# Performance work log

Measured on AMD Instinct MI355X. Metric: run time of the kernel, lower is better.

## Reference

```python
import jax, jax.numpy as jnp
import numpy as np

N_HEAD = 12

def setup_inputs() -> dict:
    key = jax.random.key(0)
    ks = jax.random.split(key, 5)
    B, T, C = 1, 4096, 768
    scale = 0.02
    return {
        "x": jax.random.normal(ks[0], (B, T, C), jnp.float32),
        "w_attn": jax.random.normal(ks[1], (C, 3 * C), jnp.float32) * scale,
        "b_attn": jax.random.normal(ks[2], (3 * C,), jnp.float32) * scale,
        "w_proj": jax.random.normal(ks[3], (C, C), jnp.float32) * scale,
        "b_proj": jax.random.normal(ks[4], (C,), jnp.float32) * scale,
    }

def reference(x, w_attn, b_attn, w_proj, b_proj):
    B, T, C = x.shape
    H = N_HEAD
    D = C // H
    qkv = x @ w_attn + b_attn                      # [B,T,3C]
    q, k, v = jnp.split(qkv, 3, axis=-1)
    # [B,T,C] -> [B,H,T,D]
    q = q.reshape(B, T, H, D).transpose(0, 2, 1, 3)
    k = k.reshape(B, T, H, D).transpose(0, 2, 1, 3)
    v = v.reshape(B, T, H, D).transpose(0, 2, 1, 3)
    att = jnp.einsum("bhqd,bhkd->bhqk", q, k) * (1.0 / np.sqrt(D))
    causal = jnp.tril(jnp.ones((T, T), bool))
    att = jnp.where(causal[None, None], att, -jnp.inf)
    att = jax.nn.softmax(att, axis=-1)
    y = jnp.einsum("bhqk,bhkd->bhqd", att, v)      # [B,H,T,D]
    y = y.transpose(0, 2, 1, 3).reshape(B, T, C)
    return y @ w_proj + b_proj
```

## Files before the change

### kernel.cpp

```cpp
#include <hip/hip_runtime.h>
#include <hip/hip_bf16.h>
#include <cstdint>
#include <cstddef>

#define NHEAD 12
#define TSEQ  4096
#define CDIM  768

typedef __attribute__((ext_vector_type(8))) short bf16x8;
typedef __attribute__((ext_vector_type(4))) float f32x4;
typedef __attribute__((ext_vector_type(16))) float f32x16;
typedef __attribute__((ext_vector_type(2))) unsigned int u32x2;

typedef __attribute__((address_space(1))) void gvoid;
typedef __attribute__((address_space(3))) void lvoid;

#define QSCALE 0.1803368801111204f

static __device__ __forceinline__ unsigned short f2bf(float f) {
    union { float f; uint32_t u; } v; v.f = f;
    uint32_t u = v.u;
    u += 0x7fffu + ((u >> 16) & 1u);
    return (unsigned short)(u >> 16);
}

static __device__ __forceinline__ f32x4 mfma16(bf16x8 a, bf16x8 b, f32x4 c) {
    return __builtin_amdgcn_mfma_f32_16x16x32_bf16(a, b, c, 0, 0, 0);
}
static __device__ __forceinline__ f32x16 mfma32(bf16x8 a, bf16x8 b, f32x16 c) {
    return __builtin_amdgcn_mfma_f32_32x32x16_bf16(a, b, c, 0, 0, 0);
}
static __device__ __forceinline__ unsigned cvt_pk_bf16(float lo, float hi) {
    unsigned r;
    asm("v_cvt_pk_bf16_f32 %0, %1, %2" : "=v"(r) : "v"(lo), "v"(hi));
    return r;
}


__global__ void cvt_f32_bf16(const float* __restrict__ in, unsigned short* __restrict__ out, int n4) {
    int i = blockIdx.x * blockDim.x + threadIdx.x;
    int stride = gridDim.x * blockDim.x;
    for (int idx = i; idx < n4; idx += stride) {
        float4 v = reinterpret_cast<const float4*>(in)[idx];
        ushort4 o;
        o.x = f2bf(v.x); o.y = f2bf(v.y); o.z = f2bf(v.z); o.w = f2bf(v.w);
        reinterpret_cast<ushort4*>(out)[idx] = o;
    }
}

__global__ void transpose_cvt(const float* __restrict__ W, unsigned short* __restrict__ Wt,
                              int K, int N) {
    __shared__ float tile[32][33];
    int n0 = blockIdx.x * 32;
    int k0 = blockIdx.y * 32;
    int tx = threadIdx.x & 31;
    int ty = threadIdx.x >> 5;
    #pragma unroll
    for (int r = ty; r < 32; r += 8)
        tile[r][tx] = W[(size_t)(k0 + r) * N + n0 + tx];
    __syncthreads();
    #pragma unroll
    for (int r = ty; r < 32; r += 8)
        Wt[(size_t)(n0 + r) * K + k0 + tx] = f2bf(tile[tx][r]);
}


template<int MODE>
__global__ __launch_bounds__(256)
void gemm_bt(const unsigned short* __restrict__ A,
             const unsigned short* __restrict__ Bt,
             const float* __restrict__ bias,
             unsigned short* __restrict__ Qb,
             unsigned short* __restrict__ Kb,
             unsigned short* __restrict__ Vt,
             float* __restrict__ Out,
             int M, int N, int K)
{
    __shared__ __align__(16) unsigned short As[128 * 32];
    __shared__ __align__(16) unsigned short Bs[128 * 32];

    const int tid  = threadIdx.x;
    const int lane = tid & 63;
    const int w    = tid >> 6;
    const int wr   = w >> 1, wc = w & 1;
    const int row0 = blockIdx.x * 128;
    const int col0 = blockIdx.y * 128;
    const int l16  = lane & 15;
    const int lhi  = lane >> 4;

    f32x4 acc[4][4] = {};

    for (int k0 = 0; k0 < K; k0 += 32) {
        __syncthreads();
        #pragma unroll
        for (int r = 0; r < 2; ++r) {
            int b    = r * 4096 + w * 1024 + lane * 16;
            int trow = b >> 6;
            int koff = b & 63;
            const char* gA = (const char*)A  + ((size_t)(row0 + trow) * K + k0) * 2 + koff;
            const char* gB = (const char*)Bt + ((size_t)(col0 + trow) * K + k0) * 2 + koff;
            __builtin_amdgcn_global_load_lds((gvoid*)gA,
                (lvoid*)((char*)As + r * 4096 + w * 1024), 16, 0, 0);
            __builtin_amdgcn_global_load_lds((gvoid*)gB,
                (lvoid*)((char*)Bs + r * 4096 + w * 1024), 16, 0, 0);
        }
        __syncthreads();

        bf16x8 a[4], bfr[4];
        #pragma unroll
        for (int m = 0; m < 4; ++m) {
            int row = wr * 64 + m * 16 + l16;
            a[m] = *reinterpret_cast<const bf16x8*>(&As[row * 32 + lhi * 8]);
        }
        #pragma unroll
        for (int n = 0; n < 4; ++n) {
            int col = wc * 64 + n * 16 + l16;
            bfr[n] = *reinterpret_cast<const bf16x8*>(&Bs[col * 32 + lhi * 8]);
        }
        #pragma unroll
        for (int m = 0; m < 4; ++m)
            #pragma unroll
            for (int n = 0; n < 4; ++n)
                acc[m][n] = mfma16(a[m], bfr[n], acc[m][n]);
    }

    #pragma unroll
    for (int m = 0; m < 4; ++m) {
        int trow = row0 + wr * 64 + m * 16 + lhi * 4;
        #pragma unroll
        for (int n = 0; n < 4; ++n) {
            int ncol = col0 + wc * 64 + n * 16 + l16;
            float bv = bias[ncol];
            #pragma unroll
            for (int j = 0; j < 4; ++j) {
                float v = acc[m][n][j] + bv;
                int t = trow + j;
                if (MODE == 0) {
                    if (ncol < 768) {
                        int hh = ncol >> 6, d = ncol & 63;
                        Qb[((size_t)hh * TSEQ + t) * 64 + d] = f2bf(v * QSCALE);
                    } else if (ncol < 1536) {
                        int c = ncol - 768; int hh = c >> 6, d = c & 63;
                        Kb[((size_t)hh * TSEQ + t) * 64 + d] = f2bf(v);
                    } else {
                        int c = ncol - 1536; int hh = c >> 6, d = c & 63;
                        Vt[((size_t)hh * 64 + d) * TSEQ + t] = f2bf(v);
                    }
                } else {
                    Out[(size_t)t * N + ncol] = v;
                }
            }
        }
    }
}


__global__ __launch_bounds__(256, 3)
void attn_fwd(const unsigned short* __restrict__ Qb,
              const unsigned short* __restrict__ Kb,
              const unsigned short* __restrict__ Vt,
              unsigned short* __restrict__ Y)
{
    __shared__ __align__(16) float Osh[3][32][64];
    __shared__ float Msh[3][64];
    __shared__ float Lsh[3][64];

    const int tid  = threadIdx.x;
    const int lane = tid & 63;
    const int w    = tid >> 6;
    const int l31  = lane & 31;
    const int hi   = lane >> 5;
    const int bid  = blockIdx.x;
    const int h    = bid % NHEAD;
    const int qb   = 127 - bid / NHEAD;
    const int q0   = qb * 32;
    const int ntiles = q0 / 64 + 1;

    const unsigned short* Qh = Qb + (size_t)h * TSEQ * 64;
    const unsigned short* Kh = Kb + (size_t)h * TSEQ * 64;
    const unsigned short* Vh = Vt + (size_t)h * 64 * TSEQ;

    bf16x8 qf[4];
    #pragma unroll
    for (int ks = 0; ks < 4; ++ks)
        qf[ks] = *reinterpret_cast<const bf16x8*>(
            &Qh[(size_t)(q0 + l31) * 64 + ks * 16 + hi * 8]);

    f32x16 o0 = {}, o1 = {};
    float mrun = -1e30f, lrun = 0.f;

    for (int kt = w; kt < ntiles; kt += 4) {
        const int kv0 = kt * 64;

        bf16x8 kf[2][4];
        #pragma unroll
        for (int sub = 0; sub < 2; ++sub)
            #pragma unroll
            for (int ks = 0; ks < 4; ++ks)
                kf[sub][ks] = *reinterpret_cast<const bf16x8*>(
                    &Kh[(size_t)(kv0 + sub * 32 + l31) * 64 + ks * 16 + hi * 8]);

        bf16x8 vf[2][4];
        #pragma unroll
        for (int d = 0; d < 2; ++d)
            #pragma unroll
            for (int ks = 0; ks < 4; ++ks)
                vf[d][ks] = *reinterpret_cast<const bf16x8*>(
                    &Vh[(size_t)(d * 32 + l31) * TSEQ + kv0 + ks * 16 + hi * 8]);

        f32x16 s0 = {}, s1 = {};
        #pragma unroll
        for (int ks = 0; ks < 4; ++ks) {
            s0 = mfma32(kf[0][ks], qf[ks], s0);
            s1 = mfma32(kf[1][ks], qf[ks], s1);
        }

        float sv[32];
        #pragma unroll
        for (int i = 0; i < 16; ++i) { sv[i] = s0[i]; sv[16 + i] = s1[i]; }

        if (kt == ntiles - 1) {
            const int qrel = q0 + l31 - kv0;
            const int h4 = hi * 4;
            #pragma unroll
            for (int i = 0; i < 32; ++i) {
                int kvbase = (i >> 4) * 32 + (i & 3) + 8 * ((i >> 2) & 3);
                if (kvbase + h4 > qrel) sv[i] = -1e30f;
            }
        }

        float t[16];
        #pragma unroll
        for (int i = 0; i < 16; ++i) t[i] = fmaxf(sv[i], sv[i + 16]);
        #pragma unroll
        for (int s = 8; s >= 1; s >>= 1)
            #pragma unroll
            for (int i = 0; i < s; ++i) t[i] = fmaxf(t[i], t[i + s]);
        float pmax;
        {
            union { float f; unsigned u; } c; c.f = t[0];
            u32x2 r = __builtin_amdgcn_permlane32_swap(c.u, c.u, false, false);
            union { unsigned u; float f; } ra, rb; ra.u = r.x; rb.u = r.y;
            pmax = fmaxf(ra.f, rb.f);
        }

        if (!__all(pmax <= mrun + 8.0f)) {
            float mnew = fmaxf(mrun, pmax);
            float corr = exp2f(mrun - mnew);
            #pragma unroll
            for (int i = 0; i < 16; ++i) { o0[i] *= corr; o1[i] *= corr; }
            lrun *= corr;
            mrun = mnew;
        }

        float e[32];
        #pragma unroll
        for (int i = 0; i < 32; ++i) e[i] = exp2f(sv[i] - mrun);

        float u[16];
        #pragma unroll
        for (int i = 0; i < 16; ++i) u[i] = e[i] + e[i + 16];
        #pragma unroll
        for (int s = 8; s >= 1; s >>= 1)
            #pragma unroll
            for (int i = 0; i < s; ++i) u[i] += u[i + s];
        float ps;
        {
            union { float f; unsigned u; } c; c.f = u[0];
            u32x2 r = __builtin_amdgcn_permlane32_swap(c.u, c.u, false, false);
            union { unsigned u; float f; } ra, rb; ra.u = r.x; rb.u = r.y;
            ps = ra.f + rb.f;
        }
        lrun += ps;

        bf16x8 pw[4];
        #pragma unroll
        for (int ks = 0; ks < 4; ++ks) {
            const int eb = (ks >> 1) * 16 + (ks & 1) * 8;
            u32x2 r02 = __builtin_amdgcn_permlane32_swap(
                cvt_pk_bf16(e[eb + 0], e[eb + 1]), cvt_pk_bf16(e[eb + 4], e[eb + 5]),
                false, false);
            u32x2 r13 = __builtin_amdgcn_permlane32_swap(
                cvt_pk_bf16(e[eb + 2], e[eb + 3]), cvt_pk_bf16(e[eb + 6], e[eb + 7]),
                false, false);
            union { unsigned wd[4]; bf16x8 v; } pk;
            pk.wd[0] = r02.x; pk.wd[1] = r13.x; pk.wd[2] = r02.y; pk.wd[3] = r13.y;
            pw[ks] = pk.v;
        }

        #pragma unroll
        for (int ks = 0; ks < 4; ++ks) {
            o0 = mfma32(vf[0][ks], pw[ks], o0);
            o1 = mfma32(vf[1][ks], pw[ks], o1);
        }
    }

    if (w > 0) {
        #pragma unroll
        for (int i = 0; i < 16; ++i) {
            Osh[w - 1][i][lane]      = o0[i];
            Osh[w - 1][16 + i][lane] = o1[i];
        }
        Msh[w - 1][lane] = mrun;
        Lsh[w - 1][lane] = lrun;
    }
    __syncthreads();
    if (w == 0) {
        #pragma unroll
        for (int p = 0; p < 3; ++p) {
            float mp = Msh[p][lane], lp = Lsh[p][lane];
            float mn = fmaxf(mrun, mp);
            float a = exp2f(mrun - mn), b = exp2f(mp - mn);
            #pragma unroll
            for (int i = 0; i < 16; ++i) {
                o0[i] = o0[i] * a + Osh[p][i][lane] * b;
                o1[i] = o1[i] * a + Osh[p][16 + i][lane] * b;
            }
            lrun = lrun * a + lp * b;
            mrun = mn;
        }

        float inv = 1.0f / lrun;
        const int trow = q0 + l31;
        #pragma unroll
        for (int d = 0; d < 2; ++d) {
            #pragma unroll
            for (int p = 0; p < 8; ++p) {
                const int rr = p * 2;
                float v0 = (d ? o1 : o0)[rr] * inv;
                float v1 = (d ? o1 : o0)[rr + 1] * inv;
                int c = h * 64 + d * 32 + (rr & 3) + 8 * (rr >> 2) + hi * 4;
                unsigned wd = cvt_pk_bf16(v0, v1);
                *reinterpret_cast<unsigned*>(
                    const_cast<unsigned short*>(&Y[(size_t)trow * CDIM + c])) = wd;
            }
        }
    }
}


extern "C" void kernel_launch(void* const* d_in, const int* in_sizes, int n_in,
                              void* d_out, int out_size, void* d_ws, size_t ws_size,
                              hipStream_t stream) {
    const float* x      = (const float*)d_in[0];
    const float* w_attn = (const float*)d_in[1];
    const float* b_attn = (const float*)d_in[2];
    const float* w_proj = (const float*)d_in[3];
    const float* b_proj = (const float*)d_in[4];
    float* out = (float*)d_out;

    char* ws = (char*)d_ws;
    unsigned short* xb  = (unsigned short*)(ws + 0);
    unsigned short* WaT = (unsigned short*)(ws + 6291456);
    unsigned short* WpT = (unsigned short*)(ws + 9830400);
    unsigned short* Qb  = (unsigned short*)(ws + 11010048);
    unsigned short* Kb  = (unsigned short*)(ws + 17301504);
    unsigned short* Vt  = (unsigned short*)(ws + 23592960);
    unsigned short* Yb  = (unsigned short*)(ws + 29884416);

    cvt_f32_bf16<<<2048, 256, 0, stream>>>(x, xb, TSEQ * CDIM / 4);
    transpose_cvt<<<dim3(2304 / 32, 768 / 32), 256, 0, stream>>>(w_attn, WaT, 768, 2304);
    transpose_cvt<<<dim3(768 / 32, 768 / 32), 256, 0, stream>>>(w_proj, WpT, 768, 768);

    gemm_bt<0><<<dim3(TSEQ / 128, 2304 / 128), 256, 0, stream>>>(
        xb, WaT, b_attn, Qb, Kb, Vt, nullptr, TSEQ, 2304, CDIM);

    attn_fwd<<<NHEAD * (TSEQ / 32), 256, 0, stream>>>(Qb, Kb, Vt, Yb);

    gemm_bt<1><<<dim3(TSEQ / 128, CDIM / 128), 256, 0, stream>>>(
        Yb, WpT, b_proj, nullptr, nullptr, nullptr, out, TSEQ, CDIM, CDIM);
}
```

Before: 231.4 us.

## Pair causal query blocks per attention workgroup and split KV across eight waves

Each attention workgroup now handles two 32-row query blocks, a long one (127-pair) and a short one (pair), so every block gets a similar amount of causal work. The grid shrinks to 768 blocks of 512 threads. Within a block the KV tiles are split across eight waves instead of four, and the partial softmax states are merged through shared memory in two stages. The aim is better load balance and more waves per KV sweep, at the cost of extra barriers, a larger shared-memory footprint, and a launch bound of 512 threads with 5 blocks that may tighten the register budget.

```diff
diff --git a/kernel.cpp b/kernel.cpp
--- a/kernel.cpp
+++ b/kernel.cpp
@@ -155,15 +155,15 @@
 }
 
 
-__global__ __launch_bounds__(256, 3)
+__global__ __launch_bounds__(512, 5)
 void attn_fwd(const unsigned short* __restrict__ Qb,
               const unsigned short* __restrict__ Kb,
               const unsigned short* __restrict__ Vt,
               unsigned short* __restrict__ Y)
 {
-    __shared__ __align__(16) float Osh[3][32][64];
-    __shared__ float Msh[3][64];
-    __shared__ float Lsh[3][64];
+    __shared__ __align__(16) float Osh[4][32][64];
+    __shared__ float Msh[4][64];
+    __shared__ float Lsh[4][64];
 
     const int tid  = threadIdx.x;
     const int lane = tid & 63;
@@ -172,167 +172,196 @@
     const int hi   = lane >> 5;
     const int bid  = blockIdx.x;
     const int h    = bid % NHEAD;
-    const int qb   = 127 - bid / NHEAD;
-    const int q0   = qb * 32;
-    const int ntiles = q0 / 64 + 1;
+    const int pair = bid / NHEAD;
 
     const unsigned short* Qh = Qb + (size_t)h * TSEQ * 64;
     const unsigned short* Kh = Kb + (size_t)h * TSEQ * 64;
     const unsigned short* Vh = Vt + (size_t)h * 64 * TSEQ;
 
-    bf16x8 qf[4];
-    #pragma unroll
-    for (int ks = 0; ks < 4; ++ks)
-        qf[ks] = *reinterpret_cast<const bf16x8*>(
-            &Qh[(size_t)(q0 + l31) * 64 + ks * 16 + hi * 8]);
-
-    f32x16 o0 = {}, o1 = {};
-    float mrun = -1e30f, lrun = 0.f;
-
-    for (int kt = w; kt < ntiles; kt += 4) {
-        const int kv0 = kt * 64;
-
-        bf16x8 kf[2][4];
-        #pragma unroll
-        for (int sub = 0; sub < 2; ++sub)
-            #pragma unroll
-            for (int ks = 0; ks < 4; ++ks)
-                kf[sub][ks] = *reinterpret_cast<const bf16x8*>(
-                    &Kh[(size_t)(kv0 + sub * 32 + l31) * 64 + ks * 16 + hi * 8]);
-
-        bf16x8 vf[2][4];
-        #pragma unroll
-        for (int d = 0; d < 2; ++d)
-            #pragma unroll
-            for (int ks = 0; ks < 4; ++ks)
-                vf[d][ks] = *reinterpret_cast<const bf16x8*>(
-                    &Vh[(size_t)(d * 32 + l31) * TSEQ + kv0 + ks * 16 + hi * 8]);
-
-        f32x16 s0 = {}, s1 = {};
-        #pragma unroll
-        for (int ks = 0; ks < 4; ++ks) {
-            s0 = mfma32(kf[0][ks], qf[ks], s0);
-            s1 = mfma32(kf[1][ks], qf[ks], s1);
-        }
-
-        float sv[32];
-        #pragma unroll
-        for (int i = 0; i < 16; ++i) { sv[i] = s0[i]; sv[16 + i] = s1[i]; }
-
-        if (kt == ntiles - 1) {
-            const int qrel = q0 + l31 - kv0;
-            const int h4 = hi * 4;
-            #pragma unroll
-            for (int i = 0; i < 32; ++i) {
-                int kvbase = (i >> 4) * 32 + (i & 3) + 8 * ((i >> 2) & 3);
-                if (kvbase + h4 > qrel) sv[i] = -1e30f;
-            }
-        }
-
-        float t[16];
-        #pragma unroll
-        for (int i = 0; i < 16; ++i) t[i] = fmaxf(sv[i], sv[i + 16]);
-        #pragma unroll
-        for (int s = 8; s >= 1; s >>= 1)
-            #pragma unroll
-            for (int i = 0; i < s; ++i) t[i] = fmaxf(t[i], t[i + s]);
-        float pmax;
-        {
-            union { float f; unsigned u; } c; c.f = t[0];
-            u32x2 r = __builtin_amdgcn_permlane32_swap(c.u, c.u, false, false);
-            union { unsigned u; float f; } ra, rb; ra.u = r.x; rb.u = r.y;
-            pmax = fmaxf(ra.f, rb.f);
-        }
-
-        if (!__all(pmax <= mrun + 8.0f)) {
-            float mnew = fmaxf(mrun, pmax);
-            float corr = exp2f(mrun - mnew);
-            #pragma unroll
-            for (int i = 0; i < 16; ++i) { o0[i] *= corr; o1[i] *= corr; }
-            lrun *= corr;
-            mrun = mnew;
-        }
-
-        float e[32];
-        #pragma unroll
-        for (int i = 0; i < 32; ++i) e[i] = exp2f(sv[i] - mrun);
-
-        float u[16];
-        #pragma unroll
-        for (int i = 0; i < 16; ++i) u[i] = e[i] + e[i + 16];
-        #pragma unroll
-        for (int s = 8; s >= 1; s >>= 1)
-            #pragma unroll
-            for (int i = 0; i < s; ++i) u[i] += u[i + s];
-        float ps;
-        {
-            union { float f; unsigned u; } c; c.f = u[0];
-            u32x2 r = __builtin_amdgcn_permlane32_swap(c.u, c.u, false, false);
-            union { unsigned u; float f; } ra, rb; ra.u = r.x; rb.u = r.y;
-            ps = ra.f + rb.f;
-        }
-        lrun += ps;
-
-        bf16x8 pw[4];
-        #pragma unroll
-        for (int ks = 0; ks < 4; ++ks) {
-            const int eb = (ks >> 1) * 16 + (ks & 1) * 8;
-            u32x2 r02 = __builtin_amdgcn_permlane32_swap(
-                cvt_pk_bf16(e[eb + 0], e[eb + 1]), cvt_pk_bf16(e[eb + 4], e[eb + 5]),
-                false, false);
-            u32x2 r13 = __builtin_amdgcn_permlane32_swap(
-                cvt_pk_bf16(e[eb + 2], e[eb + 3]), cvt_pk_bf16(e[eb + 6], e[eb + 7]),
-                false, false);
-            union { unsigned wd[4]; bf16x8 v; } pk;
-            pk.wd[0] = r02.x; pk.wd[1] = r13.x; pk.wd[2] = r02.y; pk.wd[3] = r13.y;
-            pw[ks] = pk.v;
-        }
-
-        #pragma unroll
-        for (int ks = 0; ks < 4; ++ks) {
-            o0 = mfma32(vf[0][ks], pw[ks], o0);
-            o1 = mfma32(vf[1][ks], pw[ks], o1);
-        }
-    }
-
-    if (w > 0) {
-        #pragma unroll
-        for (int i = 0; i < 16; ++i) {
-            Osh[w - 1][i][lane]      = o0[i];
-            Osh[w - 1][16 + i][lane] = o1[i];
-        }
-        Msh[w - 1][lane] = mrun;
-        Lsh[w - 1][lane] = lrun;
-    }
-    __syncthreads();
-    if (w == 0) {
-        #pragma unroll
-        for (int p = 0; p < 3; ++p) {
-            float mp = Msh[p][lane], lp = Lsh[p][lane];
+    #pragma unroll 1
+    for (int phase = 0; phase < 2; ++phase) {
+        const int qblk = phase ? pair : (127 - pair);
+        const int q0   = qblk * 32;
+        const int ntiles = q0 / 64 + 1;
+
+        bf16x8 qf[4];
+        #pragma unroll
+        for (int ks = 0; ks < 4; ++ks)
+            qf[ks] = *reinterpret_cast<const bf16x8*>(
+                &Qh[(size_t)(q0 + l31) * 64 + ks * 16 + hi * 8]);
+
+        f32x16 o0 = {}, o1 = {};
+        float mrun = -1e30f, lrun = 0.f;
+
+        for (int kt = w; kt < ntiles; kt += 8) {
+            const int kv0 = kt * 64;
+
+            bf16x8 kf[2][4];
+            #pragma unroll
+            for (int sub = 0; sub < 2; ++sub)
+                #pragma unroll
+                for (int ks = 0; ks < 4; ++ks)
+                    kf[sub][ks] = *reinterpret_cast<const bf16x8*>(
+                        &Kh[(size_t)(kv0 + sub * 32 + l31) * 64 + ks * 16 + hi * 8]);
+
+            bf16x8 vf[2][4];
+            #pragma unroll
+            for (int d = 0; d < 2; ++d)
+                #pragma unroll
+                for (int ks = 0; ks < 4; ++ks)
+                    vf[d][ks] = *reinterpret_cast<const bf16x8*>(
+                        &Vh[(size_t)(d * 32 + l31) * TSEQ + kv0 + ks * 16 + hi * 8]);
+
+            f32x16 s0 = {}, s1 = {};
+            #pragma unroll
+            for (int ks = 0; ks < 4; ++ks) {
+                s0 = mfma32(kf[0][ks], qf[ks], s0);
+                s1 = mfma32(kf[1][ks], qf[ks], s1);
+            }
+
+            float sv[32];
+            #pragma unroll
+            for (int i = 0; i < 16; ++i) { sv[i] = s0[i]; sv[16 + i] = s1[i]; }
+
+            if (kt == ntiles - 1) {
+                const int qrel = q0 + l31 - kv0;
+                const int h4 = hi * 4;
+                #pragma unroll
+                for (int i = 0; i < 32; ++i) {
+                    int kvbase = (i >> 4) * 32 + (i & 3) + 8 * ((i >> 2) & 3);
+                    if (kvbase + h4 > qrel) sv[i] = -1e30f;
+                }
+            }
+
+            float t[16];
+            #pragma unroll
+            for (int i = 0; i < 16; ++i) t[i] = fmaxf(sv[i], sv[i + 16]);
+            #pragma unroll
+            for (int s = 8; s >= 1; s >>= 1)
+                #pragma unroll
+                for (int i = 0; i < s; ++i) t[i] = fmaxf(t[i], t[i + s]);
+            float pmax;
+            {
+                union { float f; unsigned u; } c; c.f = t[0];
+                u32x2 r = __builtin_amdgcn_permlane32_swap(c.u, c.u, false, false);
+                union { unsigned u; float f; } ra, rb; ra.u = r.x; rb.u = r.y;
+                pmax = fmaxf(ra.f, rb.f);
+            }
+
+            if (!__all(pmax <= mrun + 8.0f)) {
+                float mnew = fmaxf(mrun, pmax);
+                float corr = exp2f(mrun - mnew);
+                #pragma unroll
+                for (int i = 0; i < 16; ++i) { o0[i] *= corr; o1[i] *= corr; }
+                lrun *= corr;
+                mrun = mnew;
+            }
+
+            float e[32];
+            #pragma unroll
+            for (int i = 0; i < 32; ++i) e[i] = exp2f(sv[i] - mrun);
+
+            float u[16];
+            #pragma unroll
+            for (int i = 0; i < 16; ++i) u[i] = e[i] + e[i + 16];
+            #pragma unroll
+            for (int s = 8; s >= 1; s >>= 1)
+                #pragma unroll
+                for (int i = 0; i < s; ++i) u[i] += u[i + s];
+            float ps;
+            {
+                union { float f; unsigned u; } c; c.f = u[0];
+                u32x2 r = __builtin_amdgcn_permlane32_swap(c.u, c.u, false, false);
+                union { unsigned u; float f; } ra, rb; ra.u = r.x; rb.u = r.y;
+                ps = ra.f + rb.f;
+            }
+            lrun += ps;
+
+            bf16x8 pw[4];
+            #pragma unroll
+            for (int ks = 0; ks < 4; ++ks) {
+                const int eb = (ks >> 1) * 16 + (ks & 1) * 8;
+                u32x2 r02 = __builtin_amdgcn_permlane32_swap(
+                    cvt_pk_bf16(e[eb + 0], e[eb + 1]), cvt_pk_bf16(e[eb + 4], e[eb + 5]),
+                    false, false);
+                u32x2 r13 = __builtin_amdgcn_permlane32_swap(
+                    cvt_pk_bf16(e[eb + 2], e[eb + 3]), cvt_pk_bf16(e[eb + 6], e[eb + 7]),
+                    false, false);
+                union { unsigned wd[4]; bf16x8 v; } pk;
+                pk.wd[0] = r02.x; pk.wd[1] = r13.x; pk.wd[2] = r02.y; pk.wd[3] = r13.y;
+                pw[ks] = pk.v;
+            }
+
+            #pragma unroll
+            for (int ks = 0; ks < 4; ++ks) {
+                o0 = mfma32(vf[0][ks], pw[ks], o0);
+                o1 = mfma32(vf[1][ks], pw[ks], o1);
+            }
+        }
+
+        __syncthreads();
+        if (w >= 4) {
+            #pragma unroll
+            for (int i = 0; i < 16; ++i) {
+                Osh[w - 4][i][lane]      = o0[i];
+                Osh[w - 4][16 + i][lane] = o1[i];
+            }
+            Msh[w - 4][lane] = mrun;
+            Lsh[w - 4][lane] = lrun;
+        }
+        __syncthreads();
+        if (w < 4) {
+            float mp = Msh[w][lane], lp = Lsh[w][lane];
             float mn = fmaxf(mrun, mp);
             float a = exp2f(mrun - mn), b = exp2f(mp - mn);
             #pragma unroll
             for (int i = 0; i < 16; ++i) {
-                o0[i] = o0[i] * a + Osh[p][i][lane] * b;
-                o1[i] = o1[i] * a + Osh[p][16 + i][lane] * b;
+                o0[i] = o0[i] * a + Osh[w][i][lane] * b;
+                o1[i] = o1[i] * a + Osh[w][16 + i][lane] * b;
             }
             lrun = lrun * a + lp * b;
             mrun = mn;
         }
-
-        float inv = 1.0f / lrun;
-        const int trow = q0 + l31;
-        #pragma unroll
-        for (int d = 0; d < 2; ++d) {
-            #pragma unroll
-            for (int p = 0; p < 8; ++p) {
-                const int rr = p * 2;
-                float v0 = (d ? o1 : o0)[rr] * inv;
-                float v1 = (d ? o1 : o0)[rr + 1] * inv;
-                int c = h * 64 + d * 32 + (rr & 3) + 8 * (rr >> 2) + hi * 4;
-                unsigned wd = cvt_pk_bf16(v0, v1);
-                *reinterpret_cast<unsigned*>(
-                    const_cast<unsigned short*>(&Y[(size_t)trow * CDIM + c])) = wd;
+        __syncthreads();
+        if (w >= 1 && w < 4) {
+            #pragma unroll
+            for (int i = 0; i < 16; ++i) {
+                Osh[w - 1][i][lane]      = o0[i];
+                Osh[w - 1][16 + i][lane] = o1[i];
+            }
+            Msh[w - 1][lane] = mrun;
+            Lsh[w - 1][lane] = lrun;
+        }
+        __syncthreads();
+        if (w == 0) {
+            #pragma unroll
+            for (int p = 0; p < 3; ++p) {
+                float mp = Msh[p][lane], lp = Lsh[p][lane];
+                float mn = fmaxf(mrun, mp);
+                float a = exp2f(mrun - mn), b = exp2f(mp - mn);
+                #pragma unroll
+                for (int i = 0; i < 16; ++i) {
+                    o0[i] = o0[i] * a + Osh[p][i][lane] * b;
+                    o1[i] = o1[i] * a + Osh[p][16 + i][lane] * b;
+                }
+                lrun = lrun * a + lp * b;
+                mrun = mn;
+            }
+
+            float inv = 1.0f / lrun;
+            const int trow = q0 + l31;
+            #pragma unroll
+            for (int d = 0; d < 2; ++d) {
+                #pragma unroll
+                for (int p = 0; p < 8; ++p) {
+                    const int rr = p * 2;
+                    float v0 = (d ? o1 : o0)[rr] * inv;
+                    float v1 = (d ? o1 : o0)[rr + 1] * inv;
+                    int c = h * 64 + d * 32 + (rr & 3) + 8 * (rr >> 2) + hi * 4;
+                    unsigned wd = cvt_pk_bf16(v0, v1);
+                    *reinterpret_cast<unsigned*>(
+                        const_cast<unsigned short*>(&Y[(size_t)trow * CDIM + c])) = wd;
+                }
             }
         }
     }
@@ -365,7 +394,7 @@
     gemm_bt<0><<<dim3(TSEQ / 128, 2304 / 128), 256, 0, stream>>>(
         xb, WaT, b_attn, Qb, Kb, Vt, nullptr, TSEQ, 2304, CDIM);
 
-    attn_fwd<<<NHEAD * (TSEQ / 32), 256, 0, stream>>>(Qb, Kb, Vt, Yb);
+    attn_fwd<<<NHEAD * 64, 512, 0, stream>>>(Qb, Kb, Vt, Yb);
 
     gemm_bt<1><<<dim3(TSEQ / 128, CDIM / 128), 256, 0, stream>>>(
         Yb, WpT, b_proj, nullptr, nullptr, nullptr, out, TSEQ, CDIM, CDIM);
```

Result: slower. 350.7 us (+51.6%).

## Pair causal query blocks per CTA and split KV range with separate merge kernel

Applied to the files above, without the earlier changes.

Each attention block now processes two query blocks (a long one and its mirrored short one) so causal work is balanced per CTA. When workspace allows, the KV range is also split across two CTAs, whose partial outputs (stored as bf16 with running max and sum) are combined by a new attn_merge kernel. This targets load imbalance and gives more independent CTAs at the cost of an extra launch, partial-result traffic, and bf16 rounding of the partials. The grid keeps the same total of 1536 CTAs, but each does roughly half the KV tiles of a paired load.

```diff
diff --git a/kernel.cpp b/kernel.cpp
--- a/kernel.cpp
+++ b/kernel.cpp
@@ -22,6 +22,10 @@
     uint32_t u = v.u;
     u += 0x7fffu + ((u >> 16) & 1u);
     return (unsigned short)(u >> 16);
+}
+static __device__ __forceinline__ float bf2f(unsigned short u) {
+    union { uint32_t u; float f; } v; v.u = ((uint32_t)u) << 16;
+    return v.f;
 }
 
 static __device__ __forceinline__ f32x4 mfma16(bf16x8 a, bf16x8 b, f32x4 c) {
@@ -155,11 +159,15 @@
 }
 
 
+template<int NSPLIT>
 __global__ __launch_bounds__(256, 3)
 void attn_fwd(const unsigned short* __restrict__ Qb,
               const unsigned short* __restrict__ Kb,
               const unsigned short* __restrict__ Vt,
-              unsigned short* __restrict__ Y)
+              unsigned short* __restrict__ Y,
+              unsigned short* __restrict__ PO,
+              float* __restrict__ PM,
+              float* __restrict__ PL)
 {
     __shared__ __align__(16) float Osh[3][32][64];
     __shared__ float Msh[3][64];
@@ -172,169 +180,231 @@
     const int hi   = lane >> 5;
     const int bid  = blockIdx.x;
     const int h    = bid % NHEAD;
-    const int qb   = 127 - bid / NHEAD;
-    const int q0   = qb * 32;
-    const int ntiles = q0 / 64 + 1;
+    const int rest = bid / NHEAD;
+    const int pair = rest % 64;
+    const int s    = rest / 64;
 
     const unsigned short* Qh = Qb + (size_t)h * TSEQ * 64;
     const unsigned short* Kh = Kb + (size_t)h * TSEQ * 64;
     const unsigned short* Vh = Vt + (size_t)h * 64 * TSEQ;
 
-    bf16x8 qf[4];
+    #pragma unroll 1
+    for (int phase = 0; phase < 2; ++phase) {
+        const int qblk = phase ? pair : (127 - pair);
+        const int q0   = qblk * 32;
+        const int ntiles = q0 / 64 + 1;
+
+        bf16x8 qf[4];
+        #pragma unroll
+        for (int ks = 0; ks < 4; ++ks)
+            qf[ks] = *reinterpret_cast<const bf16x8*>(
+                &Qh[(size_t)(q0 + l31) * 64 + ks * 16 + hi * 8]);
+
+        f32x16 o0 = {}, o1 = {};
+        float mrun = -1e30f, lrun = 0.f;
+
+        for (int kt = w * NSPLIT + s; kt < ntiles; kt += 4 * NSPLIT) {
+            const int kv0 = kt * 64;
+
+            bf16x8 kf[2][4];
+            #pragma unroll
+            for (int sub = 0; sub < 2; ++sub)
+                #pragma unroll
+                for (int ks = 0; ks < 4; ++ks)
+                    kf[sub][ks] = *reinterpret_cast<const bf16x8*>(
+                        &Kh[(size_t)(kv0 + sub * 32 + l31) * 64 + ks * 16 + hi * 8]);
+
+            bf16x8 vf[2][4];
+            #pragma unroll
+            for (int d = 0; d < 2; ++d)
+                #pragma unroll
+                for (int ks = 0; ks < 4; ++ks)
+                    vf[d][ks] = *reinterpret_cast<const bf16x8*>(
+                        &Vh[(size_t)(d * 32 + l31) * TSEQ + kv0 + ks * 16 + hi * 8]);
+
+            f32x16 s0 = {}, s1 = {};
+            #pragma unroll
+            for (int ks = 0; ks < 4; ++ks) {
+                s0 = mfma32(kf[0][ks], qf[ks], s0);
+                s1 = mfma32(kf[1][ks], qf[ks], s1);
+            }
+
+            float sv[32];
+            #pragma unroll
+            for (int i = 0; i < 16; ++i) { sv[i] = s0[i]; sv[16 + i] = s1[i]; }
+
+            if (kt == ntiles - 1) {
+                const int qrel = q0 + l31 - kv0;
+                const int h4 = hi * 4;
+                #pragma unroll
+                for (int i = 0; i < 32; ++i) {
+                    int kvbase = (i >> 4) * 32 + (i & 3) + 8 * ((i >> 2) & 3);
+                    if (kvbase + h4 > qrel) sv[i] = -1e30f;
+                }
+            }
+
+            float t[16];
+            #pragma unroll
+            for (int i = 0; i < 16; ++i) t[i] = fmaxf(sv[i], sv[i + 16]);
+            #pragma unroll
+            for (int ss = 8; ss >= 1; ss >>= 1)
+                #pragma unroll
+                for (int i = 0; i < ss; ++i) t[i] = fmaxf(t[i], t[i + ss]);
+            float pmax;
+            {
+                union { float f; unsigned u; } c; c.f = t[0];
+                u32x2 r = __builtin_amdgcn_permlane32_swap(c.u, c.u, false, false);
+                union { unsigned u; float f; } ra, rb; ra.u = r.x; rb.u = r.y;
+                pmax = fmaxf(ra.f, rb.f);
+            }
+
+            if (!__all(pmax <= mrun + 8.0f)) {
+                float mnew = fmaxf(mrun, pmax);
+                float corr = exp2f(mrun - mnew);
+                #pragma unroll
+                for (int i = 0; i < 16; ++i) { o0[i] *= corr; o1[i] *= corr; }
+                lrun *= corr;
+                mrun = mnew;
+            }
+
+            float e[32];
+            #pragma unroll
+            for (int i = 0; i < 32; ++i) e[i] = exp2f(sv[i] - mrun);
+
+            float u[16];
+            #pragma unroll
+            for (int i = 0; i < 16; ++i) u[i] = e[i] + e[i + 16];
+            #pragma unroll
+            for (int ss = 8; ss >= 1; ss >>= 1)
+                #pragma unroll
+                for (int i = 0; i < ss; ++i) u[i] += u[i + ss];
+            float ps;
+            {
+                union { float f; unsigned u; } c; c.f = u[0];
+                u32x2 r = __builtin_amdgcn_permlane32_swap(c.u, c.u, false, false);
+                union { unsigned u; float f; } ra, rb; ra.u = r.x; rb.u = r.y;
+                ps = ra.f + rb.f;
+            }
+            lrun += ps;
+
+            bf16x8 pw[4];
+            #pragma unroll
+            for (int ks = 0; ks < 4; ++ks) {
+                const int eb = (ks >> 1) * 16 + (ks & 1) * 8;
+                u32x2 r02 = __builtin_amdgcn_permlane32_swap(
+                    cvt_pk_bf16(e[eb + 0], e[eb + 1]), cvt_pk_bf16(e[eb + 4], e[eb + 5]),
+                    false, false);
+                u32x2 r13 = __builtin_amdgcn_permlane32_swap(
+                    cvt_pk_bf16(e[eb + 2], e[eb + 3]), cvt_pk_bf16(e[eb + 6], e[eb + 7]),
+                    false, false);
+                union { unsigned wd[4]; bf16x8 v; } pk;
+                pk.wd[0] = r02.x; pk.wd[1] = r13.x; pk.wd[2] = r02.y; pk.wd[3] = r13.y;
+                pw[ks] = pk.v;
+            }
+
+            #pragma unroll
+            for (int ks = 0; ks < 4; ++ks) {
+                o0 = mfma32(vf[0][ks], pw[ks], o0);
+                o1 = mfma32(vf[1][ks], pw[ks], o1);
+            }
+        }
+
+        __syncthreads();
+        if (w > 0) {
+            #pragma unroll
+            for (int i = 0; i < 16; ++i) {
+                Osh[w - 1][i][lane]      = o0[i];
+                Osh[w - 1][16 + i][lane] = o1[i];
+            }
+            Msh[w - 1][lane] = mrun;
+            Lsh[w - 1][lane] = lrun;
+        }
+        __syncthreads();
+        if (w == 0) {
+            #pragma unroll
+            for (int p = 0; p < 3; ++p) {
+                float mp = Msh[p][lane], lp = Lsh[p][lane];
+                float mn = fmaxf(mrun, mp);
+                float a = exp2f(mrun - mn), b = exp2f(mp - mn);
+                #pragma unroll
+                for (int i = 0; i < 16; ++i) {
+                    o0[i] = o0[i] * a + Osh[p][i][lane] * b;
+                    o1[i] = o1[i] * a + Osh[p][16 + i][lane] * b;
+                }
+                lrun = lrun * a + lp * b;
+                mrun = mn;
+            }
+
+            if constexpr (NSPLIT == 1) {
+                float inv = 1.0f / lrun;
+                const int trow = q0 + l31;
+                #pragma unroll
+                for (int d = 0; d < 2; ++d) {
+                    #pragma unroll
+                    for (int p = 0; p < 8; ++p) {
+                        const int rr = p * 2;
+                        float v0 = (d ? o1 : o0)[rr] * inv;
+                        float v1 = (d ? o1 : o0)[rr + 1] * inv;
+                        int c = h * 64 + d * 32 + (rr & 3) + 8 * (rr >> 2) + hi * 4;
+                        unsigned wd = cvt_pk_bf16(v0, v1);
+                        *reinterpret_cast<unsigned*>(
+                            const_cast<unsigned short*>(&Y[(size_t)trow * CDIM + c])) = wd;
+                    }
+                }
+            } else {
+                const int u2 = (h * 128 + qblk) * NSPLIT + s;
+                unsigned short* po = PO + (size_t)u2 * 2048;
+                #pragma unroll
+                for (int i = 0; i < 16; ++i) {
+                    po[i * 64 + lane]        = f2bf(o0[i]);
+                    po[(16 + i) * 64 + lane] = f2bf(o1[i]);
+                }
+                if (lane < 32) {
+                    PM[(size_t)u2 * 32 + lane] = mrun;
+                    PL[(size_t)u2 * 32 + lane] = lrun;
+                }
+            }
+        }
+    }
+}
+
+
+__global__ __launch_bounds__(256)
+void attn_merge(const unsigned short* __restrict__ PO,
+                const float* __restrict__ PM,
+                const float* __restrict__ PL,
+                unsigned short* __restrict__ Y)
+{
+    const int unit = blockIdx.x;
+    const int h = unit >> 7, q = unit & 127;
+    const unsigned short* p0 = PO + (size_t)unit * 2 * 2048;
+    const unsigned short* p1 = p0 + 2048;
+    const float* m01 = PM + (size_t)unit * 2 * 32;
+    const float* l01 = PL + (size_t)unit * 2 * 32;
+
     #pragma unroll
-    for (int ks = 0; ks < 4; ++ks)
-        qf[ks] = *reinterpret_cast<const bf16x8*>(
-            &Qh[(size_t)(q0 + l31) * 64 + ks * 16 + hi * 8]);
-
-    f32x16 o0 = {}, o1 = {};
-    float mrun = -1e30f, lrun = 0.f;
-
-    for (int kt = w; kt < ntiles; kt += 4) {
-        const int kv0 = kt * 64;
-
-        bf16x8 kf[2][4];
-        #pragma unroll
-        for (int sub = 0; sub < 2; ++sub)
-            #pragma unroll
-            for (int ks = 0; ks < 4; ++ks)
-                kf[sub][ks] = *reinterpret_cast<const bf16x8*>(
-                    &Kh[(size_t)(kv0 + sub * 32 + l31) * 64 + ks * 16 + hi * 8]);
-
-        bf16x8 vf[2][4];
-        #pragma unroll
-        for (int d = 0; d < 2; ++d)
-            #pragma unroll
-            for (int ks = 0; ks < 4; ++ks)
-                vf[d][ks] = *reinterpret_cast<const bf16x8*>(
-                    &Vh[(size_t)(d * 32 + l31) * TSEQ + kv0 + ks * 16 + hi * 8]);
-
-        f32x16 s0 = {}, s1 = {};
-        #pragma unroll
-        for (int ks = 0; ks < 4; ++ks) {
-            s0 = mfma32(kf[0][ks], qf[ks], s0);
-            s1 = mfma32(kf[1][ks], qf[ks], s1);
-        }
-
-        float sv[32];
-        #pragma unroll
-        for (int i = 0; i < 16; ++i) { sv[i] = s0[i]; sv[16 + i] = s1[i]; }
-
-        if (kt == ntiles - 1) {
-            const int qrel = q0 + l31 - kv0;
-            const int h4 = hi * 4;
-            #pragma unroll
-            for (int i = 0; i < 32; ++i) {
-                int kvbase = (i >> 4) * 32 + (i & 3) + 8 * ((i >> 2) & 3);
-                if (kvbase + h4 > qrel) sv[i] = -1e30f;
-            }
-        }
-
-        float t[16];
-        #pragma unroll
-        for (int i = 0; i < 16; ++i) t[i] = fmaxf(sv[i], sv[i + 16]);
-        #pragma unroll
-        for (int s = 8; s >= 1; s >>= 1)
-            #pragma unroll
-            for (int i = 0; i < s; ++i) t[i] = fmaxf(t[i], t[i + s]);
-        float pmax;
-        {
-            union { float f; unsigned u; } c; c.f = t[0];
-            u32x2 r = __builtin_amdgcn_permlane32_swap(c.u, c.u, false, false);
-            union { unsigned u; float f; } ra, rb; ra.u = r.x; rb.u = r.y;
-            pmax = fmaxf(ra.f, rb.f);
-        }
-
-        if (!__all(pmax <= mrun + 8.0f)) {
-            float mnew = fmaxf(mrun, pmax);
-            float corr = exp2f(mrun - mnew);
-            #pragma unroll
-            for (int i = 0; i < 16; ++i) { o0[i] *= corr; o1[i] *= corr; }
-            lrun *= corr;
-            mrun = mnew;
-        }
-
-        float e[32];
-        #pragma unroll
-        for (int i = 0; i < 32; ++i) e[i] = exp2f(sv[i] - mrun);
-
-        float u[16];
-        #pragma unroll
-        for (int i = 0; i < 16; ++i) u[i] = e[i] + e[i + 16];
-        #pragma unroll
-        for (int s = 8; s >= 1; s >>= 1)
-            #pragma unroll
-            for (int i = 0; i < s; ++i) u[i] += u[i + s];
-        float ps;
-        {
-            union { float f; unsigned u; } c; c.f = u[0];
-            u32x2 r = __builtin_amdgcn_permlane32_swap(c.u, c.u, false, false);
-            union { unsigned u; float f; } ra, rb; ra.u = r.x; rb.u = r.y;
-            ps = ra.f + rb.f;
-        }
-        lrun += ps;
-
-        bf16x8 pw[4];
-        #pragma unroll
-        for (int ks = 0; ks < 4; ++ks) {
-            const int eb = (ks >> 1) * 16 + (ks & 1) * 8;
-            u32x2 r02 = __builtin_amdgcn_permlane32_swap(
-                cvt_pk_bf16(e[eb + 0], e[eb + 1]), cvt_pk_bf16(e[eb + 4], e[eb + 5]),
-                false, false);
-            u32x2 r13 = __builtin_amdgcn_permlane32_swap(
-                cvt_pk_bf16(e[eb + 2], e[eb + 3]), cvt_pk_bf16(e[eb + 6], e[eb + 7]),
-                false, false);
-            union { unsigned wd[4]; bf16x8 v; } pk;
-            pk.wd[0] = r02.x; pk.wd[1] = r13.x; pk.wd[2] = r02.y; pk.wd[3] = r13.y;
-            pw[ks] = pk.v;
-        }
-
-        #pragma unroll
-        for (int ks = 0; ks < 4; ++ks) {
-            o0 = mfma32(vf[0][ks], pw[ks], o0);
-            o1 = mfma32(vf[1][ks], pw[ks], o1);
-        }
-    }
-
-    if (w > 0) {
-        #pragma unroll
-        for (int i = 0; i < 16; ++i) {
-            Osh[w - 1][i][lane]      = o0[i];
-            Osh[w - 1][16 + i][lane] = o1[i];
-        }
-        Msh[w - 1][lane] = mrun;
-        Lsh[w - 1][lane] = lrun;
-    }
-    __syncthreads();
-    if (w == 0) {
-        #pragma unroll
-        for (int p = 0; p < 3; ++p) {
-            float mp = Msh[p][lane], lp = Lsh[p][lane];
-            float mn = fmaxf(mrun, mp);
-            float a = exp2f(mrun - mn), b = exp2f(mp - mn);
-            #pragma unroll
-            for (int i = 0; i < 16; ++i) {
-                o0[i] = o0[i] * a + Osh[p][i][lane] * b;
-                o1[i] = o1[i] * a + Osh[p][16 + i][lane] * b;
-            }
-            lrun = lrun * a + lp * b;
-            mrun = mn;
-        }
-
-        float inv = 1.0f / lrun;
-        const int trow = q0 + l31;
-        #pragma unroll
-        for (int d = 0; d < 2; ++d) {
-            #pragma unroll
-            for (int p = 0; p < 8; ++p) {
-                const int rr = p * 2;
-                float v0 = (d ? o1 : o0)[rr] * inv;
-                float v1 = (d ? o1 : o0)[rr + 1] * inv;
-                int c = h * 64 + d * 32 + (rr & 3) + 8 * (rr >> 2) + hi * 4;
-                unsigned wd = cvt_pk_bf16(v0, v1);
-                *reinterpret_cast<unsigned*>(
-                    const_cast<unsigned short*>(&Y[(size_t)trow * CDIM + c])) = wd;
-            }
-        }
+    for (int i = 0; i < 4; ++i) {
+        int idx = threadIdx.x + i * 256;
+        int r  = idx >> 5;
+        int d0 = (idx & 31) * 2;
+
+        float m0 = m01[r], m1 = m01[32 + r];
+        float l0 = l01[r], l1 = l01[32 + r];
+        float mM = fmaxf(m0, m1);
+        float a = exp2f(m0 - mM), b = exp2f(m1 - mM);
+        float inv = 1.0f / (l0 * a + l1 * b);
+
+        int d5 = d0 & 31;
+        int ie = (d5 & 3) | (((d5 >> 3) & 3) << 2);
+        int hie = (d5 >> 2) & 1;
+        int e0 = ie + ((d0 >> 5) << 4);
+        int ln = r + 32 * hie;
+
+        float v0 = (bf2f(p0[e0 * 64 + ln]) * a + bf2f(p1[e0 * 64 + ln]) * b) * inv;
+        float v1 = (bf2f(p0[(e0 + 1) * 64 + ln]) * a + bf2f(p1[(e0 + 1) * 64 + ln]) * b) * inv;
+
+        unsigned wd = cvt_pk_bf16(v0, v1);
+        *reinterpret_cast<unsigned*>(&Y[(size_t)(q * 32 + r) * CDIM + h * 64 + d0]) = wd;
     }
 }
 
@@ -358,6 +428,12 @@
     unsigned short* Vt  = (unsigned short*)(ws + 23592960);
     unsigned short* Yb  = (unsigned short*)(ws + 29884416);
 
+    const size_t poOff = 36175872;
+    unsigned short* PO = (unsigned short*)(ws + poOff);
+    float* PM = (float*)(ws + poOff + 12582912);
+    float* PL = (float*)(ws + poOff + 12582912 + 393216);
+    const bool split2 = ws_size >= poOff + 12582912 + 2 * 393216;
+
     cvt_f32_bf16<<<2048, 256, 0, stream>>>(x, xb, TSEQ * CDIM / 4);
     transpose_cvt<<<dim3(2304 / 32, 768 / 32), 256, 0, stream>>>(w_attn, WaT, 768, 2304);
     transpose_cvt<<<dim3(768 / 32, 768 / 32), 256, 0, stream>>>(w_proj, WpT, 768, 768);
@@ -365,7 +441,12 @@
     gemm_bt<0><<<dim3(TSEQ / 128, 2304 / 128), 256, 0, stream>>>(
         xb, WaT, b_attn, Qb, Kb, Vt, nullptr, TSEQ, 2304, CDIM);
 
-    attn_fwd<<<NHEAD * (TSEQ / 32), 256, 0, stream>>>(Qb, Kb, Vt, Yb);
+    if (split2) {
+        attn_fwd<2><<<NHEAD * 64 * 2, 256, 0, stream>>>(Qb, Kb, Vt, Yb, PO, PM, PL);
+        attn_merge<<<NHEAD * 128, 256, 0, stream>>>(PO, PM, PL, Yb);
+    } else {
+        attn_fwd<1><<<NHEAD * 64, 256, 0, stream>>>(Qb, Kb, Vt, Yb, PO, PM, PL);
+    }
 
     gemm_bt<1><<<dim3(TSEQ / 128, CDIM / 128), 256, 0, stream>>>(
         Yb, WpT, b_proj, nullptr, nullptr, nullptr, out, TSEQ, CDIM, CDIM);
```

Measured after the change: 271.1 us. 17.2% more time.

## Pair causal query blocks per attention CTA and split V projection for coalesced transpose

Applied to the files above, without the earlier changes.

The attention kernel now runs each block over two query blocks, a long one (127-pair) and a short one (pair), so every CTA does a balanced amount of causal work. This halves the grid and evens out the tail imbalance. The QKV GEMM is split into a Q/K launch and a separate V launch. The V launch swaps the MFMA operands so its transposed Vt stores run contiguously along T, replacing the strided scatter writes. The cost is an extra kernel launch, an extra __syncthreads per phase, and less parallelism from the smaller attention grid.

```diff
diff --git a/kernel.cpp b/kernel.cpp
--- a/kernel.cpp
+++ b/kernel.cpp
@@ -120,34 +120,52 @@
         #pragma unroll
         for (int m = 0; m < 4; ++m)
             #pragma unroll
-            for (int n = 0; n < 4; ++n)
-                acc[m][n] = mfma16(a[m], bfr[n], acc[m][n]);
+            for (int n = 0; n < 4; ++n) {
+                if constexpr (MODE == 2)
+                    acc[m][n] = mfma16(bfr[n], a[m], acc[m][n]);
+                else
+                    acc[m][n] = mfma16(a[m], bfr[n], acc[m][n]);
+            }
     }
 
-    #pragma unroll
-    for (int m = 0; m < 4; ++m) {
-        int trow = row0 + wr * 64 + m * 16 + lhi * 4;
-        #pragma unroll
-        for (int n = 0; n < 4; ++n) {
-            int ncol = col0 + wc * 64 + n * 16 + l16;
-            float bv = bias[ncol];
-            #pragma unroll
-            for (int j = 0; j < 4; ++j) {
-                float v = acc[m][n][j] + bv;
-                int t = trow + j;
-                if (MODE == 0) {
-                    if (ncol < 768) {
-                        int hh = ncol >> 6, d = ncol & 63;
-                        Qb[((size_t)hh * TSEQ + t) * 64 + d] = f2bf(v * QSCALE);
-                    } else if (ncol < 1536) {
-                        int c = ncol - 768; int hh = c >> 6, d = c & 63;
-                        Kb[((size_t)hh * TSEQ + t) * 64 + d] = f2bf(v);
+    if constexpr (MODE == 2) {
+        #pragma unroll
+        for (int m = 0; m < 4; ++m) {
+            int t = row0 + wr * 64 + m * 16 + l16;
+            #pragma unroll
+            for (int n = 0; n < 4; ++n) {
+                int cb = col0 + wc * 64 + n * 16 + lhi * 4;
+                #pragma unroll
+                for (int j = 0; j < 4; ++j) {
+                    int c = cb + j;
+                    float v = acc[m][n][j] + bias[c];
+                    Vt[(size_t)c * TSEQ + t] = f2bf(v);
+                }
+            }
+        }
+    } else {
+        #pragma unroll
+        for (int m = 0; m < 4; ++m) {
+            int trow = row0 + wr * 64 + m * 16 + lhi * 4;
+            #pragma unroll
+            for (int n = 0; n < 4; ++n) {
+                int ncol = col0 + wc * 64 + n * 16 + l16;
+                float bv = bias[ncol];
+                #pragma unroll
+                for (int j = 0; j < 4; ++j) {
+                    float v = acc[m][n][j] + bv;
+                    int t = trow + j;
+                    if (MODE == 0) {
+                        if (ncol < 768) {
+                            int hh = ncol >> 6, d = ncol & 63;
+                            Qb[((size_t)hh * TSEQ + t) * 64 + d] = f2bf(v * QSCALE);
+                        } else {
+                            int c = ncol - 768; int hh = c >> 6, d = c & 63;
+                            Kb[((size_t)hh * TSEQ + t) * 64 + d] = f2bf(v);
+                        }
                     } else {
-                        int c = ncol - 1536; int hh = c >> 6, d = c & 63;
-                        Vt[((size_t)hh * 64 + d) * TSEQ + t] = f2bf(v);
+                        Out[(size_t)t * N + ncol] = v;
                     }
-                } else {
-                    Out[(size_t)t * N + ncol] = v;
                 }
             }
         }
@@ -172,167 +190,173 @@
     const int hi   = lane >> 5;
     const int bid  = blockIdx.x;
     const int h    = bid % NHEAD;
-    const int qb   = 127 - bid / NHEAD;
-    const int q0   = qb * 32;
-    const int ntiles = q0 / 64 + 1;
+    const int pair = bid / NHEAD;
 
     const unsigned short* Qh = Qb + (size_t)h * TSEQ * 64;
     const unsigned short* Kh = Kb + (size_t)h * TSEQ * 64;
     const unsigned short* Vh = Vt + (size_t)h * 64 * TSEQ;
 
-    bf16x8 qf[4];
-    #pragma unroll
-    for (int ks = 0; ks < 4; ++ks)
-        qf[ks] = *reinterpret_cast<const bf16x8*>(
-            &Qh[(size_t)(q0 + l31) * 64 + ks * 16 + hi * 8]);
-
-    f32x16 o0 = {}, o1 = {};
-    float mrun = -1e30f, lrun = 0.f;
-
-    for (int kt = w; kt < ntiles; kt += 4) {
-        const int kv0 = kt * 64;
-
-        bf16x8 kf[2][4];
-        #pragma unroll
-        for (int sub = 0; sub < 2; ++sub)
-            #pragma unroll
-            for (int ks = 0; ks < 4; ++ks)
-                kf[sub][ks] = *reinterpret_cast<const bf16x8*>(
-                    &Kh[(size_t)(kv0 + sub * 32 + l31) * 64 + ks * 16 + hi * 8]);
-
-        bf16x8 vf[2][4];
-        #pragma unroll
-        for (int d = 0; d < 2; ++d)
-            #pragma unroll
-            for (int ks = 0; ks < 4; ++ks)
-                vf[d][ks] = *reinterpret_cast<const bf16x8*>(
-                    &Vh[(size_t)(d * 32 + l31) * TSEQ + kv0 + ks * 16 + hi * 8]);
-
-        f32x16 s0 = {}, s1 = {};
-        #pragma unroll
-        for (int ks = 0; ks < 4; ++ks) {
-            s0 = mfma32(kf[0][ks], qf[ks], s0);
-            s1 = mfma32(kf[1][ks], qf[ks], s1);
-        }
-
-        float sv[32];
-        #pragma unroll
-        for (int i = 0; i < 16; ++i) { sv[i] = s0[i]; sv[16 + i] = s1[i]; }
-
-        if (kt == ntiles - 1) {
-            const int qrel = q0 + l31 - kv0;
-            const int h4 = hi * 4;
-            #pragma unroll
-            for (int i = 0; i < 32; ++i) {
-                int kvbase = (i >> 4) * 32 + (i & 3) + 8 * ((i >> 2) & 3);
-                if (kvbase + h4 > qrel) sv[i] = -1e30f;
-            }
-        }
-
-        float t[16];
-        #pragma unroll
-        for (int i = 0; i < 16; ++i) t[i] = fmaxf(sv[i], sv[i + 16]);
-        #pragma unroll
-        for (int s = 8; s >= 1; s >>= 1)
-            #pragma unroll
-            for (int i = 0; i < s; ++i) t[i] = fmaxf(t[i], t[i + s]);
-        float pmax;
-        {
-            union { float f; unsigned u; } c; c.f = t[0];
-            u32x2 r = __builtin_amdgcn_permlane32_swap(c.u, c.u, false, false);
-            union { unsigned u; float f; } ra, rb; ra.u = r.x; rb.u = r.y;
-            pmax = fmaxf(ra.f, rb.f);
-        }
-
-        if (!__all(pmax <= mrun + 8.0f)) {
-            float mnew = fmaxf(mrun, pmax);
-            float corr = exp2f(mrun - mnew);
-            #pragma unroll
-            for (int i = 0; i < 16; ++i) { o0[i] *= corr; o1[i] *= corr; }
-            lrun *= corr;
-            mrun = mnew;
-        }
-
-        float e[32];
-        #pragma unroll
-        for (int i = 0; i < 32; ++i) e[i] = exp2f(sv[i] - mrun);
-
-        float u[16];
-        #pragma unroll
-        for (int i = 0; i < 16; ++i) u[i] = e[i] + e[i + 16];
-        #pragma unroll
-        for (int s = 8; s >= 1; s >>= 1)
-            #pragma unroll
-            for (int i = 0; i < s; ++i) u[i] += u[i + s];
-        float ps;
-        {
-            union { float f; unsigned u; } c; c.f = u[0];
-            u32x2 r = __builtin_amdgcn_permlane32_swap(c.u, c.u, false, false);
-            union { unsigned u; float f; } ra, rb; ra.u = r.x; rb.u = r.y;
-            ps = ra.f + rb.f;
-        }
-        lrun += ps;
-
-        bf16x8 pw[4];
-        #pragma unroll
-        for (int ks = 0; ks < 4; ++ks) {
-            const int eb = (ks >> 1) * 16 + (ks & 1) * 8;
-            u32x2 r02 = __builtin_amdgcn_permlane32_swap(
-                cvt_pk_bf16(e[eb + 0], e[eb + 1]), cvt_pk_bf16(e[eb + 4], e[eb + 5]),
-                false, false);
-            u32x2 r13 = __builtin_amdgcn_permlane32_swap(
-                cvt_pk_bf16(e[eb + 2], e[eb + 3]), cvt_pk_bf16(e[eb + 6], e[eb + 7]),
-                false, false);
-            union { unsigned wd[4]; bf16x8 v; } pk;
-            pk.wd[0] = r02.x; pk.wd[1] = r13.x; pk.wd[2] = r02.y; pk.wd[3] = r13.y;
-            pw[ks] = pk.v;
-        }
-
-        #pragma unroll
-        for (int ks = 0; ks < 4; ++ks) {
-            o0 = mfma32(vf[0][ks], pw[ks], o0);
-            o1 = mfma32(vf[1][ks], pw[ks], o1);
-        }
-    }
-
-    if (w > 0) {
-        #pragma unroll
-        for (int i = 0; i < 16; ++i) {
-            Osh[w - 1][i][lane]      = o0[i];
-            Osh[w - 1][16 + i][lane] = o1[i];
-        }
-        Msh[w - 1][lane] = mrun;
-        Lsh[w - 1][lane] = lrun;
-    }
-    __syncthreads();
-    if (w == 0) {
-        #pragma unroll
-        for (int p = 0; p < 3; ++p) {
-            float mp = Msh[p][lane], lp = Lsh[p][lane];
-            float mn = fmaxf(mrun, mp);
-            float a = exp2f(mrun - mn), b = exp2f(mp - mn);
+    #pragma unroll 1
+    for (int phase = 0; phase < 2; ++phase) {
+        const int qblk = phase ? pair : (127 - pair);
+        const int q0   = qblk * 32;
+        const int ntiles = q0 / 64 + 1;
+
+        bf16x8 qf[4];
+        #pragma unroll
+        for (int ks = 0; ks < 4; ++ks)
+            qf[ks] = *reinterpret_cast<const bf16x8*>(
+                &Qh[(size_t)(q0 + l31) * 64 + ks * 16 + hi * 8]);
+
+        f32x16 o0 = {}, o1 = {};
+        float mrun = -1e30f, lrun = 0.f;
+
+        for (int kt = w; kt < ntiles; kt += 4) {
+            const int kv0 = kt * 64;
+
+            bf16x8 kf[2][4];
+            #pragma unroll
+            for (int sub = 0; sub < 2; ++sub)
+                #pragma unroll
+                for (int ks = 0; ks < 4; ++ks)
+                    kf[sub][ks] = *reinterpret_cast<const bf16x8*>(
+                        &Kh[(size_t)(kv0 + sub * 32 + l31) * 64 + ks * 16 + hi * 8]);
+
+            bf16x8 vf[2][4];
+            #pragma unroll
+            for (int d = 0; d < 2; ++d)
+                #pragma unroll
+                for (int ks = 0; ks < 4; ++ks)
+                    vf[d][ks] = *reinterpret_cast<const bf16x8*>(
+                        &Vh[(size_t)(d * 32 + l31) * TSEQ + kv0 + ks * 16 + hi * 8]);
+
+            f32x16 s0 = {}, s1 = {};
+            #pragma unroll
+            for (int ks = 0; ks < 4; ++ks) {
+                s0 = mfma32(kf[0][ks], qf[ks], s0);
+                s1 = mfma32(kf[1][ks], qf[ks], s1);
+            }
+
+            float sv[32];
+            #pragma unroll
+            for (int i = 0; i < 16; ++i) { sv[i] = s0[i]; sv[16 + i] = s1[i]; }
+
+            if (kt == ntiles - 1) {
+                const int qrel = q0 + l31 - kv0;
+                const int h4 = hi * 4;
+                #pragma unroll
+                for (int i = 0; i < 32; ++i) {
+                    int kvbase = (i >> 4) * 32 + (i & 3) + 8 * ((i >> 2) & 3);
+                    if (kvbase + h4 > qrel) sv[i] = -1e30f;
+                }
+            }
+
+            float t[16];
+            #pragma unroll
+            for (int i = 0; i < 16; ++i) t[i] = fmaxf(sv[i], sv[i + 16]);
+            #pragma unroll
+            for (int ss = 8; ss >= 1; ss >>= 1)
+                #pragma unroll
+                for (int i = 0; i < ss; ++i) t[i] = fmaxf(t[i], t[i + ss]);
+            float pmax;
+            {
+                union { float f; unsigned u; } c; c.f = t[0];
+                u32x2 r = __builtin_amdgcn_permlane32_swap(c.u, c.u, false, false);
+                union { unsigned u; float f; } ra, rb; ra.u = r.x; rb.u = r.y;
+                pmax = fmaxf(ra.f, rb.f);
+            }
+
+            if (!__all(pmax <= mrun + 8.0f)) {
+                float mnew = fmaxf(mrun, pmax);
+                float corr = exp2f(mrun - mnew);
+                #pragma unroll
+                for (int i = 0; i < 16; ++i) { o0[i] *= corr; o1[i] *= corr; }
+                lrun *= corr;
+                mrun = mnew;
+            }
+
+            float e[32];
+            #pragma unroll
+            for (int i = 0; i < 32; ++i) e[i] = exp2f(sv[i] - mrun);
+
+            float u[16];
+            #pragma unroll
+            for (int i = 0; i < 16; ++i) u[i] = e[i] + e[i + 16];
+            #pragma unroll
+            for (int ss = 8; ss >= 1; ss >>= 1)
+                #pragma unroll
+                for (int i = 0; i < ss; ++i) u[i] += u[i + ss];
+            float ps;
+            {
+                union { float f; unsigned u; } c; c.f = u[0];
+                u32x2 r = __builtin_amdgcn_permlane32_swap(c.u, c.u, false, false);
+                union { unsigned u; float f; } ra, rb; ra.u = r.x; rb.u = r.y;
+                ps = ra.f + rb.f;
+            }
+            lrun += ps;
+
+            bf16x8 pw[4];
+            #pragma unroll
+            for (int ks = 0; ks < 4; ++ks) {
+                const int eb = (ks >> 1) * 16 + (ks & 1) * 8;
+                u32x2 r02 = __builtin_amdgcn_permlane32_swap(
+                    cvt_pk_bf16(e[eb + 0], e[eb + 1]), cvt_pk_bf16(e[eb + 4], e[eb + 5]),
+                    false, false);
+                u32x2 r13 = __builtin_amdgcn_permlane32_swap(
+                    cvt_pk_bf16(e[eb + 2], e[eb + 3]), cvt_pk_bf16(e[eb + 6], e[eb + 7]),
+                    false, false);
+                union { unsigned wd[4]; bf16x8 v; } pk;
+                pk.wd[0] = r02.x; pk.wd[1] = r13.x; pk.wd[2] = r02.y; pk.wd[3] = r13.y;
+                pw[ks] = pk.v;
+            }
+
+            #pragma unroll
+            for (int ks = 0; ks < 4; ++ks) {
+                o0 = mfma32(vf[0][ks], pw[ks], o0);
+                o1 = mfma32(vf[1][ks], pw[ks], o1);
+            }
+        }
+
+        __syncthreads();
+        if (w > 0) {
             #pragma unroll
             for (int i = 0; i < 16; ++i) {
-                o0[i] = o0[i] * a + Osh[p][i][lane] * b;
-                o1[i] = o1[i] * a + Osh[p][16 + i][lane] * b;
-            }
-            lrun = lrun * a + lp * b;
-            mrun = mn;
-        }
-
-        float inv = 1.0f / lrun;
-        const int trow = q0 + l31;
-        #pragma unroll
-        for (int d = 0; d < 2; ++d) {
-            #pragma unroll
-            for (int p = 0; p < 8; ++p) {
-                const int rr = p * 2;
-                float v0 = (d ? o1 : o0)[rr] * inv;
-                float v1 = (d ? o1 : o0)[rr + 1] * inv;
-                int c = h * 64 + d * 32 + (rr & 3) + 8 * (rr >> 2) + hi * 4;
-                unsigned wd = cvt_pk_bf16(v0, v1);
-                *reinterpret_cast<unsigned*>(
-                    const_cast<unsigned short*>(&Y[(size_t)trow * CDIM + c])) = wd;
+                Osh[w - 1][i][lane]      = o0[i];
+                Osh[w - 1][16 + i][lane] = o1[i];
+            }
+            Msh[w - 1][lane] = mrun;
+            Lsh[w - 1][lane] = lrun;
+        }
+        __syncthreads();
+        if (w == 0) {
+            #pragma unroll
+            for (int p = 0; p < 3; ++p) {
+                float mp = Msh[p][lane], lp = Lsh[p][lane];
+                float mn = fmaxf(mrun, mp);
+                float a = exp2f(mrun - mn), b = exp2f(mp - mn);
+                #pragma unroll
+                for (int i = 0; i < 16; ++i) {
+                    o0[i] = o0[i] * a + Osh[p][i][lane] * b;
+                    o1[i] = o1[i] * a + Osh[p][16 + i][lane] * b;
+                }
+                lrun = lrun * a + lp * b;
+                mrun = mn;
+            }
+
+            float inv = 1.0f / lrun;
+            const int trow = q0 + l31;
+            #pragma unroll
+            for (int d = 0; d < 2; ++d) {
+                #pragma unroll
+                for (int p = 0; p < 8; ++p) {
+                    const int rr = p * 2;
+                    float v0 = (d ? o1 : o0)[rr] * inv;
+                    float v1 = (d ? o1 : o0)[rr + 1] * inv;
+                    int c = h * 64 + d * 32 + (rr & 3) + 8 * (rr >> 2) + hi * 4;
+                    unsigned wd = cvt_pk_bf16(v0, v1);
+                    *reinterpret_cast<unsigned*>(
+                        const_cast<unsigned short*>(&Y[(size_t)trow * CDIM + c])) = wd;
+                }
             }
         }
     }
@@ -362,10 +386,13 @@
     transpose_cvt<<<dim3(2304 / 32, 768 / 32), 256, 0, stream>>>(w_attn, WaT, 768, 2304);
     transpose_cvt<<<dim3(768 / 32, 768 / 32), 256, 0, stream>>>(w_proj, WpT, 768, 768);
 
-    gemm_bt<0><<<dim3(TSEQ / 128, 2304 / 128), 256, 0, stream>>>(
-        xb, WaT, b_attn, Qb, Kb, Vt, nullptr, TSEQ, 2304, CDIM);
-
-    attn_fwd<<<NHEAD * (TSEQ / 32), 256, 0, stream>>>(Qb, Kb, Vt, Yb);
+    gemm_bt<0><<<dim3(TSEQ / 128, 1536 / 128), 256, 0, stream>>>(
+        xb, WaT, b_attn, Qb, Kb, nullptr, nullptr, TSEQ, 2304, CDIM);
+    gemm_bt<2><<<dim3(TSEQ / 128, 768 / 128), 256, 0, stream>>>(
+        xb, WaT + (size_t)1536 * 768, b_attn + 1536, nullptr, nullptr, Vt, nullptr,
+        TSEQ, 768, CDIM);
+
+    attn_fwd<<<NHEAD * 64, 256, 0, stream>>>(Qb, Kb, Vt, Yb);
 
     gemm_bt<1><<<dim3(TSEQ / 128, CDIM / 128), 256, 0, stream>>>(
         Yb, WpT, b_proj, nullptr, nullptr, nullptr, out, TSEQ, CDIM, CDIM);
```

New measurement: 243.0 us. +5.1%, slower.
